# Kernel optimization log

Hardware: AMD Instinct MI355X
Metric: run time of the kernel (lower is better)

The kernel has to match this reference:

```python
import jax, jax.numpy as jnp
import numpy as np

B, L, D, N, V = 32, 4096, 128, 5, 128  # batch, seq, embed dim, n-gram order, alphabet size


def setup_inputs() -> dict:
    key = jax.random.key(0)
    k1, k2, k3 = jax.random.split(key, 3)
    x = jax.random.randint(k1, (B, L), 0, V, dtype=jnp.int32)
    emb = jax.random.normal(k2, (V, D), dtype=jnp.float32)
    W = jax.random.normal(k3, (V, D * (N - 1)), dtype=jnp.float32) * 0.05
    b = jnp.zeros((V,), dtype=jnp.float32)
    return {"x": x, "emb": emb, "W": W, "b": b}


def reference(x, emb, W, b):
    n1 = N - 1  # context window size
    x_enc = emb[x]  # (B, L, D) embedding gather
    # enc[:, j, k*D:(k+1)*D] = x_enc[:, j - n1 + k] for j >= n1; zeros for j < n1.
    # Build each slot by right-shifting the embedded sequence by (n1 - k).
    Lcur = x.shape[1]
    parts = [jnp.pad(x_enc, ((0, 0), (n1 - k, 0), (0, 0)))[:, :Lcur] for k in range(n1)]
    enc = jnp.concatenate(parts, axis=-1)  # (B, L, n1*D)
    valid = (jnp.arange(Lcur) >= n1)[None, :, None]
    enc = jnp.where(valid, enc, jnp.zeros((), enc.dtype))
    # linear: logits = enc @ W^T + b  -> (B, L, V)
    logits = jnp.einsum("blf,vf->blv", enc, W) + b
    return logits
```

## Files before the change

kernel.cpp:

```cpp
#include <hip/hip_runtime.h>

constexpr int Bn = 32;
constexpr int Ln = 4096;
constexpr int Dn = 128;
constexpr int Vn = 128;
constexpr int N1 = 4;

typedef float vfloat4 __attribute__((ext_vector_type(4)));

__global__ void build_table_kernel(const float* __restrict__ emb,
                                   const float* __restrict__ W,
                                   const float* __restrict__ bias,
                                   float* __restrict__ T) {
    const int kt = blockIdx.x;
    const int k  = kt >> 7;
    const int t  = kt & 127;
    const int v  = threadIdx.x;

    __shared__ float4 e[Dn / 4];
    if (threadIdx.x < Dn / 4) {
        e[threadIdx.x] = ((const float4*)(emb + t * Dn))[threadIdx.x];
    }
    __syncthreads();

    const float4* w = (const float4*)(W + (size_t)v * (Dn * N1) + k * Dn);
    float acc = (k == 0) ? bias[v] : 0.f;
#pragma unroll
    for (int i = 0; i < Dn / 4; ++i) {
        float4 wv = w[i];
        float4 ev = e[i];
        acc += wv.x * ev.x + wv.y * ev.y + wv.z * ev.z + wv.w * ev.w;
    }
    T[(size_t)kt * Vn + v] = acc;
}

__global__ void __launch_bounds__(256)
ngram_logits_kernel(const int* __restrict__ x,
                    const float* __restrict__ T,
                    const float* __restrict__ bias,
                    float* __restrict__ out) {
    const int tid     = blockIdx.x * blockDim.x + threadIdx.x;
    const int vq      = tid & 31;
    const int g       = tid >> 5;
    const int basepos = g << 2;
    const int j0      = basepos & (Ln - 1);

    vfloat4* outq = (vfloat4*)out;

    if (j0 == 0) {
        const vfloat4 bv = ((const vfloat4*)bias)[vq];
#pragma unroll
        for (int i = 0; i < 4; ++i)
            __builtin_nontemporal_store(bv, &outq[(size_t)(basepos + i) * 32 + vq]);
        return;
    }

    const int4 xa = *(const int4*)(x + basepos - 4);
    const int4 xb = *(const int4*)(x + basepos);
    int w[7] = {xa.x, xa.y, xa.z, xa.w, xb.x, xb.y, xb.z};

    const vfloat4* Tq = (const vfloat4*)T;
    vfloat4 acc[4];
#pragma unroll
    for (int i = 0; i < 4; ++i) {
        vfloat4 a = Tq[(size_t)(0 * Vn + w[i + 0]) * 32 + vq];
#pragma unroll
        for (int k = 1; k < N1; ++k) {
            a += Tq[(size_t)(k * Vn + w[i + k]) * 32 + vq];
        }
        acc[i] = a;
    }

#pragma unroll
    for (int i = 0; i < 4; ++i)
        __builtin_nontemporal_store(acc[i], &outq[(size_t)(basepos + i) * 32 + vq]);
}

extern "C" void kernel_launch(void* const* d_in, const int* in_sizes, int n_in,
                              void* d_out, int out_size, void* d_ws, size_t ws_size,
                              hipStream_t stream) {
    const int*   x    = (const int*)d_in[0];
    const float* emb  = (const float*)d_in[1];
    const float* W    = (const float*)d_in[2];
    const float* bias = (const float*)d_in[3];
    float*       out  = (float*)d_out;
    float*       T    = (float*)d_ws;

    build_table_kernel<<<N1 * Vn, Vn, 0, stream>>>(emb, W, bias, T);

    const int total_threads = (Bn * Ln / 4) * (Vn / 4);
    const int block = 256;
    ngram_logits_kernel<<<total_threads / block, block, 0, stream>>>(x, T, bias, out);
}
```

Before: 92.52 us.

## Rewrite table build with wave-level shuffle reductions and drop nontemporal stores

The table-build kernel now uses 256 threads per block, one wave per 32 output columns. Each lane holds two embedding elements and the dot product is reduced with xor shuffles, replacing the per-thread serial loop over strided W rows. This gives coalesced W reads. Separately, the main kernel's nontemporal stores become ordinary float4 stores, which changes the cache behaviour of the 64 MB output write and may hurt streaming throughput.

```diff
diff --git a/kernel.cpp b/kernel.cpp
--- a/kernel.cpp
+++ b/kernel.cpp
@@ -6,32 +6,29 @@
 constexpr int Vn = 128;
 constexpr int N1 = 4;
 
-typedef float vfloat4 __attribute__((ext_vector_type(4)));
+__global__ void __launch_bounds__(256)
+build_table_kernel(const float* __restrict__ emb,
+                   const float* __restrict__ W,
+                   const float* __restrict__ bias,
+                   float* __restrict__ T) {
+    const int kt   = blockIdx.x;
+    const int k    = kt >> 7;
+    const int t    = kt & 127;
+    const int wave = threadIdx.x >> 6;
+    const int lane = threadIdx.x & 63;
 
-__global__ void build_table_kernel(const float* __restrict__ emb,
-                                   const float* __restrict__ W,
-                                   const float* __restrict__ bias,
-                                   float* __restrict__ T) {
-    const int kt = blockIdx.x;
-    const int k  = kt >> 7;
-    const int t  = kt & 127;
-    const int v  = threadIdx.x;
+    const float2 e2 = *(const float2*)(emb + t * Dn + lane * 2);
 
-    __shared__ float4 e[Dn / 4];
-    if (threadIdx.x < Dn / 4) {
-        e[threadIdx.x] = ((const float4*)(emb + t * Dn))[threadIdx.x];
+    for (int vp = 0; vp < 32; ++vp) {
+        const int v = (wave << 5) | vp;
+        const float2 w2 = *(const float2*)(W + (size_t)v * (Dn * N1) + k * Dn + lane * 2);
+        float p = w2.x * e2.x + w2.y * e2.y;
+#pragma unroll
+        for (int m = 1; m < 64; m <<= 1)
+            p += __shfl_xor(p, m, 64);
+        if (lane == 0)
+            T[kt * Vn + v] = p + (k == 0 ? bias[v] : 0.f);
     }
-    __syncthreads();
-
-    const float4* w = (const float4*)(W + (size_t)v * (Dn * N1) + k * Dn);
-    float acc = (k == 0) ? bias[v] : 0.f;
-#pragma unroll
-    for (int i = 0; i < Dn / 4; ++i) {
-        float4 wv = w[i];
-        float4 ev = e[i];
-        acc += wv.x * ev.x + wv.y * ev.y + wv.z * ev.z + wv.w * ev.w;
-    }
-    T[(size_t)kt * Vn + v] = acc;
 }
 
 __global__ void __launch_bounds__(256)
@@ -45,13 +42,13 @@
     const int basepos = g << 2;
     const int j0      = basepos & (Ln - 1);
 
-    vfloat4* outq = (vfloat4*)out;
+    float4* outq = (float4*)out;
 
     if (j0 == 0) {
-        const vfloat4 bv = ((const vfloat4*)bias)[vq];
+        const float4 bv = ((const float4*)bias)[vq];
 #pragma unroll
         for (int i = 0; i < 4; ++i)
-            __builtin_nontemporal_store(bv, &outq[(size_t)(basepos + i) * 32 + vq]);
+            outq[(size_t)(basepos + i) * 32 + vq] = bv;
         return;
     }
 
@@ -59,21 +56,22 @@
     const int4 xb = *(const int4*)(x + basepos);
     int w[7] = {xa.x, xa.y, xa.z, xa.w, xb.x, xb.y, xb.z};
 
-    const vfloat4* Tq = (const vfloat4*)T;
-    vfloat4 acc[4];
+    const float4* Tq = (const float4*)T;
+    float4 acc[4];
 #pragma unroll
     for (int i = 0; i < 4; ++i) {
-        vfloat4 a = Tq[(size_t)(0 * Vn + w[i + 0]) * 32 + vq];
+        float4 a = Tq[(size_t)(0 * Vn + w[i + 0]) * 32 + vq];
 #pragma unroll
         for (int k = 1; k < N1; ++k) {
-            a += Tq[(size_t)(k * Vn + w[i + k]) * 32 + vq];
+            const float4 tk = Tq[(size_t)(k * Vn + w[i + k]) * 32 + vq];
+            a.x += tk.x; a.y += tk.y; a.z += tk.z; a.w += tk.w;
         }
         acc[i] = a;
     }
 
 #pragma unroll
     for (int i = 0; i < 4; ++i)
-        __builtin_nontemporal_store(acc[i], &outq[(size_t)(basepos + i) * 32 + vq]);
+        outq[(size_t)(basepos + i) * 32 + vq] = acc[i];
 }
 
 extern "C" void kernel_launch(void* const* d_in, const int* in_sizes, int n_in,
@@ -86,7 +84,7 @@
     float*       out  = (float*)d_out;
     float*       T    = (float*)d_ws;
 
-    build_table_kernel<<<N1 * Vn, Vn, 0, stream>>>(emb, W, bias, T);
+    build_table_kernel<<<N1 * Vn, 256, 0, stream>>>(emb, W, bias, T);
 
     const int total_threads = (Bn * Ln / 4) * (Vn / 4);
     const int block = 256;
```

New measurement: 105.3 us. 13.8% more time.
